# Kernel tuning notes

Hardware: AMD Instinct MI355X
Metric: run time of the kernel (lower is better)

Reference implementation:

```python
import jax, jax.numpy as jnp
import numpy as np

NUM_HEADS = 8
GROUP = 16
LN_EPS = 1e-5

def _star_relu(x, scale, bias):
    return scale * jnp.square(jax.nn.relu(x)) + bias

def _layernorm(x, w, b):
    mu = x.mean(-1, keepdims=True)
    var = jnp.mean(jnp.square(x - mu), -1, keepdims=True)
    return (x - mu) / jnp.sqrt(var + LN_EPS) * w + b

def _attention(x, qkv_w, proj_w, proj_b, pa_scale, pa_bias, lf_w, lf_b, hf_w, hf_b, lf_gamma, hf_gamma):
    B, N, C = x.shape
    hd = C // NUM_HEADS
    detail = _star_relu(x, pa_scale, pa_bias)
    lf = jnp.tanh(detail @ lf_w.T + lf_b)                      # (B,N,H)
    hf = jax.nn.softplus(detail @ hf_w.T + hf_b)
    hf_sq = jnp.square(hf)
    hf = 2.0 * hf_sq / (hf_sq + 0.3678)
    lf = jnp.repeat(lf, hd, axis=-1)                           # (B,N,C): per-head value repeated across head_dim
    hf = jnp.repeat(hf, hd, axis=-1)
    qkv = (x @ qkv_w.T).reshape(B, N, 3, NUM_HEADS, hd).transpose(2, 0, 3, 1, 4)
    q, k, v = qkv[0], qkv[1], qkv[2]
    q = q * (hd ** -0.5)
    attn = jax.nn.softmax(jnp.einsum('bhqd,bhkd->bhqk', q, k), axis=-1)
    attn_out = jnp.einsum('bhqk,bhkd->bhqd', attn, v).transpose(0, 2, 1, 3).reshape(B, N, C)
    value_tokens = v.transpose(0, 2, 1, 3).reshape(B, N, C)
    high_res = value_tokens - attn_out
    attn_out = attn_out + attn_out * lf * lf_gamma + hf * high_res * hf_gamma
    return attn_out @ proj_w.T + proj_b

def _freq_scale(x, rw1_w, rw1_scale, rw1_bias, rw2_w, freq_w):
    # x: (B,C,H,W); freq_w: (num_filters, C//group, base_size, base_size//2+1) == rfft grid
    B, C, H, W = x.shape
    xf = jnp.fft.rfft2(x, axes=(2, 3), norm='ortho')           # (B,C,fh,fw) complex
    pooled = x.mean(axis=(2, 3))                               # (B,C)
    h = _star_relu(pooled @ rw1_w.T, rw1_scale, rw1_bias)
    routing = jnp.tanh((h @ rw2_w.T).reshape(B, GROUP, -1))    # (B,g,f)
    fh, fw = xf.shape[2], xf.shape[3]
    dyn = jnp.einsum('bgf,fchw->bgchw', routing, freq_w).reshape(B, C, fh, fw)
    xf = xf * dyn
    return jnp.fft.irfft2(xf, s=(H, W), axes=(2, 3), norm='ortho')

def _forward(x, norm1_w, norm1_b, qkv_w, proj_w, proj_b, pa_scale, pa_bias, lf_w, lf_b, hf_w, hf_b,
             lf_gamma, hf_gamma, fs1_rw1_w, fs1_rw1_scale, fs1_rw1_bias, fs1_rw2_w, fs1_fw, gamma_1,
             norm2_w, norm2_b, fc1_w, fc1_b, fc2_w, fc2_b, fs2_rw1_w, fs2_rw1_scale, fs2_rw1_bias,
             fs2_rw2_w, fs2_fw, gamma_2):
    B, C, H, W = x.shape
    tokens = x.reshape(B, C, H * W).transpose(0, 2, 1)         # nchw -> nlc
    att_tokens = _attention(_layernorm(tokens, norm1_w, norm1_b),
                            qkv_w, proj_w, proj_b, pa_scale, pa_bias,
                            lf_w, lf_b, hf_w, hf_b, lf_gamma, hf_gamma)
    att_feat = att_tokens.transpose(0, 2, 1).reshape(B, C, H, W)
    att_feat = _freq_scale(att_feat, fs1_rw1_w, fs1_rw1_scale, fs1_rw1_bias, fs1_rw2_w, fs1_fw) + att_feat
    att_tokens = att_feat.reshape(B, C, H * W).transpose(0, 2, 1)
    tokens = tokens + gamma_1 * att_tokens
    h = _layernorm(tokens, norm2_w, norm2_b)
    mlp_tokens = jax.nn.gelu(h @ fc1_w.T + fc1_b, approximate=False) @ fc2_w.T + fc2_b
    mlp_feat = mlp_tokens.transpose(0, 2, 1).reshape(B, C, H, W)
    mlp_feat = _freq_scale(mlp_feat, fs2_rw1_w, fs2_rw1_scale, fs2_rw1_bias, fs2_rw2_w, fs2_fw) + mlp_feat
    mlp_tokens = mlp_feat.reshape(B, C, H * W).transpose(0, 2, 1)
    tokens = tokens + gamma_2 * mlp_tokens
    return tokens.transpose(0, 2, 1).reshape(B, C, H, W)

def setup_inputs() -> dict:
    key = jax.random.key(0)
    ks = jax.random.split(key, 16)
    B, C, H, W = 16, 512, 32, 32
    heads, group, nf, bs = 8, 16, 4, 32
    hid_rw = int(C * 0.125)
    hid_mlp = int(C * 4.0)
    bfs = bs // 2 + 1
    d = {}
    d['x'] = jax.random.normal(ks[0], (B, C, H, W), jnp.float32)
    d['norm1_w'] = jnp.ones((C,), jnp.float32); d['norm1_b'] = jnp.zeros((C,), jnp.float32)
    d['qkv_w'] = jax.random.normal(ks[1], (3 * C, C), jnp.float32) * 0.02
    d['proj_w'] = jax.random.normal(ks[2], (C, C), jnp.float32) * 0.02
    d['proj_b'] = jnp.zeros((C,), jnp.float32)
    d['pa_scale'] = jnp.ones((1,), jnp.float32); d['pa_bias'] = jnp.zeros((1,), jnp.float32)
    d['lf_w'] = jax.random.normal(ks[3], (heads, C), jnp.float32) * 0.02
    d['lf_b'] = jnp.zeros((heads,), jnp.float32)
    d['hf_w'] = jax.random.normal(ks[4], (heads, C), jnp.float32) * 0.02
    d['hf_b'] = jnp.zeros((heads,), jnp.float32)
    d['lf_gamma'] = 1e-5 * jnp.ones((C,), jnp.float32)
    d['hf_gamma'] = 1e-5 * jnp.ones((C,), jnp.float32)
    d['fs1_rw1_w'] = jax.random.normal(ks[5], (hid_rw, C), jnp.float32) * 0.02
    d['fs1_rw1_scale'] = jnp.ones((1,), jnp.float32); d['fs1_rw1_bias'] = jnp.zeros((1,), jnp.float32)
    d['fs1_rw2_w'] = jax.random.normal(ks[6], (group * nf, hid_rw), jnp.float32) * 0.02
    d['fs1_fw'] = jax.random.normal(ks[7], (nf, C // group, bs, bfs), jnp.float32) * 1e-5
    d['gamma_1'] = 1e-4 * jnp.ones((C,), jnp.float32)
    d['norm2_w'] = jnp.ones((C,), jnp.float32); d['norm2_b'] = jnp.zeros((C,), jnp.float32)
    d['fc1_w'] = jax.random.normal(ks[8], (hid_mlp, C), jnp.float32) * 0.02
    d['fc1_b'] = jnp.zeros((hid_mlp,), jnp.float32)
    d['fc2_w'] = jax.random.normal(ks[9], (C, hid_mlp), jnp.float32) * 0.02
    d['fc2_b'] = jnp.zeros((C,), jnp.float32)
    d['fs2_rw1_w'] = jax.random.normal(ks[10], (hid_rw, C), jnp.float32) * 0.02
    d['fs2_rw1_scale'] = jnp.ones((1,), jnp.float32); d['fs2_rw1_bias'] = jnp.zeros((1,), jnp.float32)
    d['fs2_rw2_w'] = jax.random.normal(ks[11], (group * nf, hid_rw), jnp.float32) * 0.02
    d['fs2_fw'] = jax.random.normal(ks[12], (nf, C // group, bs, bfs), jnp.float32) * 1e-5
    d['gamma_2'] = 1e-4 * jnp.ones((C,), jnp.float32)
    return d

def reference(x, norm1_w, norm1_b, qkv_w, proj_w, proj_b, pa_scale, pa_bias, lf_w, lf_b, hf_w, hf_b,
              lf_gamma, hf_gamma, fs1_rw1_w, fs1_rw1_scale, fs1_rw1_bias, fs1_rw2_w, fs1_fw, gamma_1,
              norm2_w, norm2_b, fc1_w, fc1_b, fc2_w, fc2_b, fs2_rw1_w, fs2_rw1_scale, fs2_rw1_bias,
              fs2_rw2_w, fs2_fw, gamma_2):
    return _forward(x, norm1_w, norm1_b, qkv_w, proj_w, proj_b, pa_scale, pa_bias, lf_w, lf_b, hf_w, hf_b,
                    lf_gamma, hf_gamma, fs1_rw1_w, fs1_rw1_scale, fs1_rw1_bias, fs1_rw2_w, fs1_fw, gamma_1,
                    norm2_w, norm2_b, fc1_w, fc1_b, fc2_w, fc2_b, fs2_rw1_w, fs2_rw1_scale, fs2_rw1_bias,
                    fs2_rw2_w, fs2_fw, gamma_2)
```

## Files before the change

kernel.cpp:

```cpp
#include <hip/hip_runtime.h>
#include <cstdint>
#include <cstddef>

#define B_   16
#define C_   512
#define N_   1024
#define M_   (B_*N_)
#define NH_  8
#define HD_  64
#define C3_  1536
#define CH_  2048

typedef __attribute__((ext_vector_type(8))) short bf16x8;
typedef __attribute__((ext_vector_type(4))) float f32x4;
typedef __attribute__((ext_vector_type(4))) unsigned short u16x4;

__device__ __forceinline__ unsigned short f2bf(float f) {
  union { float f; unsigned u; } v; v.f = f;
  unsigned r = v.u + 0x7fffu + ((v.u >> 16) & 1u);
  return (unsigned short)(r >> 16);
}
__device__ __forceinline__ float bf2f(unsigned short h) {
  union { unsigned u; float f; } v; v.u = ((unsigned)h) << 16;
  return v.f;
}
__device__ __forceinline__ unsigned f2u(float f) {
  union { float f; unsigned u; } v; v.f = f; return v.u;
}

#define GL16(gp, lp) \
  __builtin_amdgcn_global_load_lds( \
      (const __attribute__((address_space(1))) unsigned int*)(const void*)(gp), \
      (__attribute__((address_space(3))) unsigned int*)(void*)(lp), 16, 0, 0)

__global__ __launch_bounds__(256) void k_f2b4(
    const float* __restrict__ s0, unsigned short* __restrict__ d0,
    const float* __restrict__ s1, unsigned short* __restrict__ d1,
    const float* __restrict__ s2, unsigned short* __restrict__ d2,
    const float* __restrict__ s3, unsigned short* __restrict__ d3) {
  int blk = blockIdx.x, t = threadIdx.x;
  const float* s; unsigned short* d; int off;
  if (blk < 3072)      { s = s0; d = d0; off = blk * 256; }
  else if (blk < 4096) { s = s1; d = d1; off = (blk - 3072) * 256; }
  else if (blk < 8192) { s = s2; d = d2; off = (blk - 4096) * 256; }
  else                 { s = s3; d = d3; off = (blk - 8192) * 256; }
  int i = off + t;
  d[i] = f2bf(s[i]);
}

__global__ __launch_bounds__(256) void k_twid(unsigned short* __restrict__ gtab) {
  int idx = blockIdx.x * 256 + threadIdx.x;
  if (idx >= 6400) return;
  int tab = idx / 1280, rem = idx % 1280;
  int i = rem / 40, j = rem % 40;
  float v = 0.f;
  if (j < 32) {
    float th = 0.19634954084936207f * (float)((i * j) & 31);
    float s, c;
    __sincosf(th, &s, &c);
    if (tab == 0) v = c;
    else if (tab == 1) v = s;
    else if (tab == 2) v = -s;
    else {
      float wg = (j == 0 || j == 16) ? 1.f : 2.f;
      if (j >= 17) wg = 0.f;
      v = (tab == 3) ? wg * c : -wg * s;
    }
  }
  gtab[idx] = f2bf(v);
}

template<bool WITH>
__global__ __launch_bounds__(256) void k_lnt(const float* __restrict__ src,
    const float* __restrict__ w, const float* __restrict__ bia,
    const float* __restrict__ lfw, const float* __restrict__ lfb,
    const float* __restrict__ hfw, const float* __restrict__ hfb,
    const float* __restrict__ pa_s, const float* __restrict__ pa_b,
    unsigned short* __restrict__ lnout, float* __restrict__ lfout,
    float* __restrict__ hfout) {
  __shared__ unsigned short s[512 * 34];
  const int t = threadIdx.x, wv = t >> 6, l = t & 63;
  const int n0 = blockIdx.x * 32, b = blockIdx.y;
  const int cl = t >> 3;
  const int nn = (t & 7) * 4;
  #pragma unroll
  for (int k = 0; k < 16; ++k) {
    int c = k * 32 + cl;
    float4 v = *(const float4*)&src[(size_t)(b * C_ + c) * N_ + n0 + nn];
    s[c * 34 + nn]     = f2bf(v.x);
    s[c * 34 + nn + 1] = f2bf(v.y);
    s[c * 34 + nn + 2] = f2bf(v.z);
    s[c * 34 + nn + 3] = f2bf(v.w);
  }
  __syncthreads();
  float wv8[8], bv8[8];
  #pragma unroll
  for (int k = 0; k < 8; ++k) { wv8[k] = w[l + 64 * k]; bv8[k] = bia[l + 64 * k]; }
  float ps = 1.f, pb = 0.f;
  if (WITH) { ps = pa_s[0]; pb = pa_b[0]; }
  for (int ri = 0; ri < 8; ++ri) {
    const int n = wv * 8 + ri;
    const int row = b * N_ + n0 + n;
    float v[8];
    #pragma unroll
    for (int k = 0; k < 8; ++k) v[k] = bf2f(s[(l + 64 * k) * 34 + n]);
    float sm = 0.f, q = 0.f;
    #pragma unroll
    for (int k = 0; k < 8; ++k) { sm += v[k]; q += v[k] * v[k]; }
    #pragma unroll
    for (int off = 1; off < 64; off <<= 1) { sm += __shfl_xor(sm, off); q += __shfl_xor(q, off); }
    float mu = sm * (1.f / 512.f);
    float var = q * (1.f / 512.f) - mu * mu;
    float rstd = rsqrtf(var + 1e-5f);
    float ln[8];
    #pragma unroll
    for (int k = 0; k < 8; ++k) ln[k] = (v[k] - mu) * rstd * wv8[k] + bv8[k];
    #pragma unroll
    for (int k = 0; k < 8; ++k)
      lnout[(size_t)row * C_ + l + 64 * k] = f2bf(ln[k]);
    if (WITH) {
      float d[8];
      #pragma unroll
      for (int k = 0; k < 8; ++k) { float r = fmaxf(ln[k], 0.f); d[k] = ps * r * r + pb; }
      float lacc[8], hacc[8];
      #pragma unroll
      for (int h = 0; h < 8; ++h) {
        float la = 0.f, ha = 0.f;
        #pragma unroll
        for (int k = 0; k < 8; ++k) {
          la += d[k] * lfw[h * C_ + l + 64 * k];
          ha += d[k] * hfw[h * C_ + l + 64 * k];
        }
        lacc[h] = la; hacc[h] = ha;
      }
      #pragma unroll
      for (int h = 0; h < 8; ++h)
        #pragma unroll
        for (int off = 1; off < 64; off <<= 1) {
          lacc[h] += __shfl_xor(lacc[h], off);
          hacc[h] += __shfl_xor(hacc[h], off);
        }
      float lv = lacc[0], hv = hacc[0];
      #pragma unroll
      for (int h = 1; h < 8; ++h) { if (l == h) { lv = lacc[h]; hv = hacc[h]; } }
      if (l < 8) {
        lfout[(size_t)row * 8 + l] = tanhf(lv + lfb[l]);
        float z = hv + hfb[l];
        float sp = (z > 15.f) ? z : log1pf(__expf(z));
        float s2 = sp * sp;
        hfout[(size_t)row * 8 + l] = 2.f * s2 / (s2 + 0.3678f);
      }
    }
  }
}

template<int EPI>
__global__ __launch_bounds__(256) void k_gemm(const unsigned short* __restrict__ A,
    const unsigned short* __restrict__ Bt, const float* __restrict__ bias,
    void* __restrict__ outv, unsigned short* __restrict__ vtg, int Nn, int K, int nx) {
  __shared__ __align__(16) unsigned short Asm[128 * 32];
  __shared__ __align__(16) unsigned short Bsm[128 * 32];
  const int t = threadIdx.x, w = t >> 6, l = t & 63;
  const int lane15 = l & 15, quad = l >> 4;
  const int cpx = gridDim.x >> 3;
  const int wgs = (blockIdx.x & 7) * cpx + (blockIdx.x >> 3);
  const int bx = wgs % nx, by = wgs / nx;
  const int n0 = bx * 128, m0 = by * 128;
  const int wm = w >> 1, wn = w & 1;
  f32x4 acc[4][4];
  #pragma unroll
  for (int i = 0; i < 4; ++i)
    #pragma unroll
    for (int j = 0; j < 4; ++j) acc[i][j] = (f32x4){0.f, 0.f, 0.f, 0.f};
  const int srow = w * 16 + (l >> 2);
  const int scol = (l & 3) * 8;
  const unsigned short* gA = A + (size_t)(m0 + srow) * K + scol;
  const unsigned short* gB = Bt + (size_t)(n0 + srow) * K + scol;
  const size_t rk64 = (size_t)64 * K;
  char* lA0 = (char*)Asm + w * 1024;
  char* lA1 = (char*)Asm + 4096 + w * 1024;
  char* lB0 = (char*)Bsm + w * 1024;
  char* lB1 = (char*)Bsm + 4096 + w * 1024;
  for (int k0 = 0; k0 < K; k0 += 32) {
    __syncthreads();
    GL16(gA + k0, lA0);
    GL16(gA + k0 + rk64, lA1);
    GL16(gB + k0, lB0);
    GL16(gB + k0 + rk64, lB1);
    __syncthreads();
    bf16x8 af[4], bg[4];
    #pragma unroll
    for (int i = 0; i < 4; ++i)
      af[i] = *(const bf16x8*)&Asm[(wm * 64 + i * 16 + lane15) * 32 + quad * 8];
    #pragma unroll
    for (int i = 0; i < 4; ++i)
      bg[i] = *(const bf16x8*)&Bsm[(wn * 64 + i * 16 + lane15) * 32 + quad * 8];
    #pragma unroll
    for (int i = 0; i < 4; ++i)
      #pragma unroll
      for (int j = 0; j < 4; ++j)
        acc[i][j] = __builtin_amdgcn_mfma_f32_16x16x32_bf16(af[i], bg[j], acc[i][j], 0, 0, 0);
  }
  #pragma unroll
  for (int i = 0; i < 4; ++i) {
    int grow = m0 + wm * 64 + i * 16 + quad * 4;
    int bq = grow >> 10, nq = grow & 1023;
    #pragma unroll
    for (int j = 0; j < 4; ++j) {
      int gcol = n0 + wn * 64 + j * 16 + lane15;
      float bs = (EPI == 0) ? 0.f : bias[gcol];
      if (EPI == 1 || EPI == 3) {
        float4 o = make_float4(acc[i][j][0] + bs, acc[i][j][1] + bs,
                               acc[i][j][2] + bs, acc[i][j][3] + bs);
        *(float4*)&((float*)outv)[((size_t)(bq * C_ + gcol) << 10) + nq] = o;
      } else if (EPI == 0) {
        u16x4 pv;
        #pragma unroll
        for (int r = 0; r < 4; ++r) {
          unsigned short hv = f2bf(acc[i][j][r]);
          pv[r] = hv;
          ((unsigned short*)outv)[(size_t)(grow + r) * Nn + gcol] = hv;
        }
        if (gcol >= 1024)
          *(u16x4*)&vtg[((size_t)(bq * C_ + gcol - 1024) << 10) + nq] = pv;
      } else {
        #pragma unroll
        for (int r = 0; r < 4; ++r) {
          float vv = acc[i][j][r] + bs;
          float e = __builtin_amdgcn_exp2f(-(2.302118073f * vv +
                                             0.1029455568f * vv * vv * vv));
          float g = vv * __builtin_amdgcn_rcpf(1.f + e);
          ((unsigned short*)outv)[(size_t)(grow + r) * Nn + gcol] = f2bf(g);
        }
      }
    }
  }
}

__global__ __launch_bounds__(256, 4) void k_flash(const unsigned short* __restrict__ qkv,
    const unsigned short* __restrict__ vtg, const float* __restrict__ lf,
    const float* __restrict__ hf, const float* __restrict__ lgam,
    const float* __restrict__ hgam, unsigned short* __restrict__ y) {
  const int t = threadIdx.x, w = t >> 6, l = t & 63;
  const int lane15 = l & 15, quad = l >> 4;
  const int wg = (blockIdx.x & 7) * 128 + (blockIdx.x >> 3);
  const int qt = wg & 7;
  const int h = (wg >> 3) & 7;
  const int b = wg >> 6;
  const int q0 = qt * 128;

  __shared__ __align__(16) unsigned short kt[64 * 64];
  __shared__ __align__(16) unsigned short vt[64 * 64];
  __shared__ __align__(16) unsigned short pl[4][16 * 72];

  bf16x8 aq[2][2];
  #pragma unroll
  for (int qh = 0; qh < 2; ++qh) {
    const unsigned short* qp = qkv +
        (size_t)(b * N_ + q0 + w * 32 + qh * 16 + lane15) * C3_ + h * 64 + quad * 8;
    bf16x8 r0 = *(const bf16x8*)qp;
    bf16x8 r1 = *(const bf16x8*)(qp + 32);
    #pragma unroll
    for (int i = 0; i < 8; ++i) {
      aq[qh][0][i] = (short)f2bf(0.1803368801111713f * bf2f((unsigned short)r0[i]));
      aq[qh][1][i] = (short)f2bf(0.1803368801111713f * bf2f((unsigned short)r1[i]));
    }
  }
  f32x4 O[2][4];
  #pragma unroll
  for (int qh = 0; qh < 2; ++qh)
    #pragma unroll
    for (int i = 0; i < 4; ++i) O[qh][i] = (f32x4){0.f, 0.f, 0.f, 0.f};
  float lsum[2] = {0.f, 0.f};

  const int prow = w * 8 + (l >> 3);
  const int csw = ((l & 7) ^ (l >> 3)) * 8;
  const unsigned short* kg = qkv + (size_t)(b * N_ + prow) * C3_ + 512 + h * 64 + csw;
  const unsigned short* vg = vtg + (size_t)((b * NH_ + h) * HD_ + prow) * N_ + csw;
  char* ktb0 = (char*)kt + w * 1024;
  char* ktb1 = (char*)kt + 4096 + w * 1024;
  char* vtb0 = (char*)vt + w * 1024;
  char* vtb1 = (char*)vt + 4096 + w * 1024;
  const int swx = (lane15 & 7) * 8;

  for (int kti = 0; kti < 16; ++kti) {
    __syncthreads();
    const unsigned short* kr = kg + (size_t)(kti * 64) * C3_;
    GL16(kr, ktb0);
    GL16(kr + (size_t)32 * C3_, ktb1);
    const unsigned short* vr = vg + kti * 64;
    GL16(vr, vtb0);
    GL16(vr + 32 * N_, vtb1);
    __syncthreads();

    #pragma unroll
    for (int qh = 0; qh < 2; ++qh) {
      f32x4 S[4];
      __builtin_amdgcn_s_setprio(1);
      #pragma unroll
      for (int nt = 0; nt < 4; ++nt) {
        const int nrow = nt * 16 + lane15;
        bf16x8 ak0 = *(const bf16x8*)&kt[nrow * 64 + ((quad * 8) ^ swx)];
        bf16x8 ak1 = *(const bf16x8*)&kt[nrow * 64 + ((32 + quad * 8) ^ swx)];
        f32x4 z = (f32x4){0.f, 0.f, 0.f, 0.f};
        z = __builtin_amdgcn_mfma_f32_16x16x32_bf16(ak0, aq[qh][0], z, 0, 0, 0);
        z = __builtin_amdgcn_mfma_f32_16x16x32_bf16(ak1, aq[qh][1], z, 0, 0, 0);
        S[nt] = z;
      }
      __builtin_amdgcn_s_setprio(0);
      #pragma unroll
      for (int nt = 0; nt < 4; ++nt)
        #pragma unroll
        for (int r = 0; r < 4; ++r) {
          float pv = __builtin_amdgcn_exp2f(S[nt][r]);
          S[nt][r] = pv;
          lsum[qh] += pv;
        }
      #pragma unroll
      for (int nt = 0; nt < 4; ++nt) {
        unsigned lo = __builtin_amdgcn_perm(f2u(S[nt][1]), f2u(S[nt][0]), 0x07060302u);
        unsigned hi = __builtin_amdgcn_perm(f2u(S[nt][3]), f2u(S[nt][2]), 0x07060302u);
        *(uint2*)&pl[w][lane15 * 72 + nt * 16 + quad * 4] = make_uint2(lo, hi);
      }
      __builtin_amdgcn_s_setprio(1);
      #pragma unroll
      for (int nc = 0; nc < 2; ++nc) {
        bf16x8 ap = *(const bf16x8*)&pl[w][lane15 * 72 + nc * 32 + quad * 8];
        #pragma unroll
        for (int dt = 0; dt < 4; ++dt) {
          const int vrow = dt * 16 + lane15;
          bf16x8 bv = *(const bf16x8*)&vt[vrow * 64 + ((nc * 32 + quad * 8) ^ swx)];
          O[qh][dt] = __builtin_amdgcn_mfma_f32_16x16x32_bf16(ap, bv, O[qh][dt], 0, 0, 0);
        }
      }
      __builtin_amdgcn_s_setprio(0);
    }
  }

  #pragma unroll
  for (int qh = 0; qh < 2; ++qh) {
    float s = lsum[qh];
    s += __shfl_xor(s, 16);
    s += __shfl_xor(s, 32);
    float inv = 1.f / s;
    float invr[4], lfr[4], hfr[4];
    const size_t rowb = (size_t)(b * N_ + q0 + w * 32 + qh * 16 + quad * 4);
    #pragma unroll
    for (int r = 0; r < 4; ++r) {
      invr[r] = __shfl(inv, quad * 4 + r);
      lfr[r] = lf[(rowb + r) * 8 + h];
      hfr[r] = hf[(rowb + r) * 8 + h];
    }
    #pragma unroll
    for (int dt = 0; dt < 4; ++dt) {
      const int cc = h * 64 + dt * 16 + lane15;
      const float lg = lgam[cc], hg = hgam[cc];
      #pragma unroll
      for (int r = 0; r < 4; ++r) {
        float a = O[qh][dt][r] * invr[r];
        float vval = bf2f(qkv[(rowb + r) * C3_ + 1024 + cc]);
        float res = a + a * lfr[r] * lg + hfr[r] * (vval - a) * hg;
        y[(rowb + r) * C_ + cc] = f2bf(res);
      }
    }
  }
}

__global__ __launch_bounds__(256) void k_pool(const float* __restrict__ feat,
                                              float* __restrict__ pooled) {
  int row = blockIdx.x * 4 + (threadIdx.x >> 6);
  int l = threadIdx.x & 63;
  const float4* p = (const float4*)(feat + (size_t)row * N_);
  float4 a = p[l], b4 = p[l + 64], c4 = p[l + 128], d4 = p[l + 192];
  float s = a.x + a.y + a.z + a.w + b4.x + b4.y + b4.z + b4.w +
            c4.x + c4.y + c4.z + c4.w + d4.x + d4.y + d4.z + d4.w;
  #pragma unroll
  for (int off = 1; off < 64; off <<= 1) s += __shfl_xor(s, off);
  if (l == 0) pooled[row] = s * (1.f / 1024.f);
}

__global__ __launch_bounds__(256) void k_routing(const float* __restrict__ pooled,
    const float* __restrict__ rw1, const float* __restrict__ rw1s,
    const float* __restrict__ rw1b, const float* __restrict__ rw2,
    float* __restrict__ routing) {
  const int b = blockIdx.x, t = threadIdx.x;
  __shared__ float plds[512];
  __shared__ float tile[64][65];
  __shared__ float hl[64];
  plds[t] = pooled[b * 512 + t];
  plds[t + 256] = pooled[b * 512 + t + 256];
  __syncthreads();
  float acc = 0.f;
  for (int c0 = 0; c0 < 512; c0 += 64) {
    #pragma unroll
    for (int kk = 0; kk < 16; ++kk) {
      int idx = kk * 256 + t;
      tile[idx >> 6][idx & 63] = rw1[(size_t)(idx >> 6) * 512 + c0 + (idx & 63)];
    }
    __syncthreads();
    if (t < 64) {
      #pragma unroll
      for (int i = 0; i < 64; ++i) acc += plds[c0 + i] * tile[t][i];
    }
    __syncthreads();
  }
  if (t < 64) {
    float r = fmaxf(acc, 0.f);
    hl[t] = rw1s[0] * r * r + rw1b[0];
  }
  __syncthreads();
  if (t < 64) {
    float r2 = 0.f;
    #pragma unroll
    for (int j = 0; j < 64; ++j) r2 += hl[j] * rw2[(size_t)t * 64 + j];
    routing[b * 64 + t] = tanhf(r2);
  }
}

__global__ __launch_bounds__(256) void k_freq(const float* __restrict__ feat,
    const float* __restrict__ routing, const float* __restrict__ fwtab,
    const unsigned short* __restrict__ gtab, const float* __restrict__ res,
    const float* __restrict__ gamma, float* __restrict__ outp) {
  const int c = blockIdx.x, b = blockIdx.y, t = threadIdx.x;
  const int g = c >> 5, cc = c & 31;
  const int w = t >> 6, l = t & 63;
  const int lane15 = l & 15, quad = l >> 4;
  const int mt = w & 1, nt = w >> 1;
  __shared__ __align__(16) unsigned short Xbf[32 * 40];
  __shared__ __align__(16) float p[32 * 36];
  __shared__ __align__(16) unsigned short Tabs[6400];
  __shared__ __align__(16) unsigned short pl1r[32 * 40], pl1i[32 * 40];
  __shared__ __align__(16) unsigned short pl2r[32 * 40], pl2i[32 * 40];
  __shared__ __align__(16) unsigned short pl3r[32 * 40], pl3i[32 * 40];
  __shared__ float Ms[1024];
  const size_t base = (size_t)(b * C_ + c) * N_;

  {
    float4 v = ((const float4*)(feat + base))[t];
    int hh = t >> 3, w4 = (t & 7) * 4;
    *(float4*)&p[hh * 36 + w4] = v;
    u16x4 xb = { f2bf(v.x), f2bf(v.y), f2bf(v.z), f2bf(v.w) };
    *(u16x4*)&Xbf[hh * 40 + w4] = xb;
  }
  {
    const uint4* src = (const uint4*)gtab;
    uint4* dst = (uint4*)Tabs;
    #pragma unroll
    for (int k = 0; k < 4; ++k) {
      int o = k * 256 + t;
      if (o < 800) dst[o] = src[o];
    }
  }
  {
    float r0 = routing[b * 64 + g * 4 + 0];
    float r1 = routing[b * 64 + g * 4 + 1];
    float r2 = routing[b * 64 + g * 4 + 2];
    float r3 = routing[b * 64 + g * 4 + 3];
    const float* fb = fwtab + (size_t)cc * 544;
    #pragma unroll
    for (int k = 0; k < 4; ++k) {
      int o = k * 256 + t;
      int fh = o >> 5, fw = o & 31;
      float mv = 0.f;
      if (fw < 17) {
        int fi = fh * 17 + fw;
        mv = (r0 * fb[fi] + r1 * fb[17408 + fi] + r2 * fb[34816 + fi] +
              r3 * fb[52224 + fi]) * (1.f / 1024.f);
      }
      Ms[o] = mv;
    }
  }
  __syncthreads();

  const unsigned short* Tc  = Tabs;
  const unsigned short* Ts  = Tabs + 1280;
  const unsigned short* Tsn = Tabs + 2560;
  const unsigned short* Tcw = Tabs + 3840;
  const unsigned short* Tsw = Tabs + 5120;
  const int arow = (mt * 16 + lane15) * 40 + quad * 8;
  const int brow = (nt * 16 + lane15) * 40 + quad * 8;
  const int prow = (nt * 16 + lane15) * 40 + mt * 16 + quad * 4;
  const f32x4 zz = (f32x4){0.f, 0.f, 0.f, 0.f};

  {
    bf16x8 aX = *(const bf16x8*)&Xbf[arow];
    bf16x8 bC = *(const bf16x8*)&Tc[brow];
    bf16x8 bS = *(const bf16x8*)&Tsn[brow];
    f32x4 re = __builtin_amdgcn_mfma_f32_16x16x32_bf16(aX, bC, zz, 0, 0, 0);
    f32x4 im = __builtin_amdgcn_mfma_f32_16x16x32_bf16(aX, bS, zz, 0, 0, 0);
    uint2 pr = make_uint2(__builtin_amdgcn_perm(f2u(re[1]), f2u(re[0]), 0x07060302u),
                          __builtin_amdgcn_perm(f2u(re[3]), f2u(re[2]), 0x07060302u));
    uint2 pi = make_uint2(__builtin_amdgcn_perm(f2u(im[1]), f2u(im[0]), 0x07060302u),
                          __builtin_amdgcn_perm(f2u(im[3]), f2u(im[2]), 0x07060302u));
    *(uint2*)&pl1r[prow] = pr;
    *(uint2*)&pl1i[prow] = pi;
  }
  __syncthreads();
  {
    bf16x8 aC = *(const bf16x8*)&Tc[arow];
    bf16x8 aS = *(const bf16x8*)&Ts[arow];
    bf16x8 aN = *(const bf16x8*)&Tsn[arow];
    bf16x8 bR = *(const bf16x8*)&pl1r[brow];
    bf16x8 bI = *(const bf16x8*)&pl1i[brow];
    f32x4 er = __builtin_amdgcn_mfma_f32_16x16x32_bf16(aC, bR, zz, 0, 0, 0);
    er = __builtin_amdgcn_mfma_f32_16x16x32_bf16(aS, bI, er, 0, 0, 0);
    f32x4 ei = __builtin_amdgcn_mfma_f32_16x16x32_bf16(aC, bI, zz, 0, 0, 0);
    ei = __builtin_amdgcn_mfma_f32_16x16x32_bf16(aN, bR, ei, 0, 0, 0);
    #pragma unroll
    for (int r = 0; r < 4; ++r) {
      float mk = Ms[(mt * 16 + quad * 4 + r) * 32 + nt * 16 + lane15];
      er[r] *= mk; ei[r] *= mk;
    }
    uint2 pr = make_uint2(__builtin_amdgcn_perm(f2u(er[1]), f2u(er[0]), 0x07060302u),
                          __builtin_amdgcn_perm(f2u(er[3]), f2u(er[2]), 0x07060302u));
    uint2 pi = make_uint2(__builtin_amdgcn_perm(f2u(ei[1]), f2u(ei[0]), 0x07060302u),
                          __builtin_amdgcn_perm(f2u(ei[3]), f2u(ei[2]), 0x07060302u));
    *(uint2*)&pl2r[prow] = pr;
    *(uint2*)&pl2i[prow] = pi;
  }
  __syncthreads();
  {
    bf16x8 aR = *(const bf16x8*)&pl2r[arow];
    bf16x8 aI = *(const bf16x8*)&pl2i[arow];
    bf16x8 bC = *(const bf16x8*)&Tc[brow];
    bf16x8 bS = *(const bf16x8*)&Ts[brow];
    bf16x8 bN = *(const bf16x8*)&Tsn[brow];
    f32x4 zr = __builtin_amdgcn_mfma_f32_16x16x32_bf16(aR, bC, zz, 0, 0, 0);
    zr = __builtin_amdgcn_mfma_f32_16x16x32_bf16(aI, bN, zr, 0, 0, 0);
    f32x4 zi = __builtin_amdgcn_mfma_f32_16x16x32_bf16(aI, bC, zz, 0, 0, 0);
    zi = __builtin_amdgcn_mfma_f32_16x16x32_bf16(aR, bS, zi, 0, 0, 0);
    uint2 pr = make_uint2(__builtin_amdgcn_perm(f2u(zr[1]), f2u(zr[0]), 0x07060302u),
                          __builtin_amdgcn_perm(f2u(zr[3]), f2u(zr[2]), 0x07060302u));
    uint2 pi = make_uint2(__builtin_amdgcn_perm(f2u(zi[1]), f2u(zi[0]), 0x07060302u),
                          __builtin_amdgcn_perm(f2u(zi[3]), f2u(zi[2]), 0x07060302u));
    *(uint2*)&pl3r[prow] = pr;
    *(uint2*)&pl3i[prow] = pi;
  }
  __syncthreads();
  {
    bf16x8 aC = *(const bf16x8*)&Tcw[arow];
    bf16x8 aS = *(const bf16x8*)&Tsw[arow];
    bf16x8 bR = *(const bf16x8*)&pl3r[brow];
    bf16x8 bI = *(const bf16x8*)&pl3i[brow];
    f32x4 y = __builtin_amdgcn_mfma_f32_16x16x32_bf16(aC, bR, zz, 0, 0, 0);
    y = __builtin_amdgcn_mfma_f32_16x16x32_bf16(aS, bI, y, 0, 0, 0);
    int hh = nt * 16 + lane15, w0 = mt * 16 + quad * 4;
    float4 fp = *(const float4*)&p[hh * 36 + w0];
    float4 rp = *(const float4*)&res[base + hh * 32 + w0];
    float gv = gamma[c];
    float4 o = make_float4(rp.x + gv * (y[0] + fp.x), rp.y + gv * (y[1] + fp.y),
                           rp.z + gv * (y[2] + fp.z), rp.w + gv * (y[3] + fp.w));
    *(float4*)&outp[base + hh * 32 + w0] = o;
  }
}

extern "C" void kernel_launch(void* const* d_in, const int* in_sizes, int n_in,
                              void* d_out, int out_size, void* d_ws, size_t ws_size,
                              hipStream_t stream) {
  (void)in_sizes; (void)n_in; (void)out_size; (void)ws_size;
  const float* x      = (const float*)d_in[0];
  const float* n1w    = (const float*)d_in[1];
  const float* n1b    = (const float*)d_in[2];
  const float* qkv_w  = (const float*)d_in[3];
  const float* proj_w = (const float*)d_in[4];
  const float* proj_b = (const float*)d_in[5];
  const float* pa_s   = (const float*)d_in[6];
  const float* pa_b   = (const float*)d_in[7];
  const float* lf_w   = (const float*)d_in[8];
  const float* lf_b   = (const float*)d_in[9];
  const float* hf_w   = (const float*)d_in[10];
  const float* hf_b   = (const float*)d_in[11];
  const float* lf_g   = (const float*)d_in[12];
  const float* hf_g   = (const float*)d_in[13];
  const float* f1rw1w = (const float*)d_in[14];
  const float* f1rw1s = (const float*)d_in[15];
  const float* f1rw1b = (const float*)d_in[16];
  const float* f1rw2w = (const float*)d_in[17];
  const float* f1fw   = (const float*)d_in[18];
  const float* gamma1 = (const float*)d_in[19];
  const float* n2w    = (const float*)d_in[20];
  const float* n2b    = (const float*)d_in[21];
  const float* fc1w   = (const float*)d_in[22];
  const float* fc1b   = (const float*)d_in[23];
  const float* fc2w   = (const float*)d_in[24];
  const float* fc2b   = (const float*)d_in[25];
  const float* f2rw1w = (const float*)d_in[26];
  const float* f2rw1s = (const float*)d_in[27];
  const float* f2rw1b = (const float*)d_in[28];
  const float* f2rw2w = (const float*)d_in[29];
  const float* f2fw   = (const float*)d_in[30];
  const float* gamma2 = (const float*)d_in[31];

  char* ws = (char*)d_ws;
  float*          tokens = (float*)(ws + 0);
  float*          f1buf  = (float*)(ws + 33554432ULL);
  float*          f2buf  = (float*)(ws + 67108864ULL);
  unsigned short* regA   = (unsigned short*)(ws + 134217728ULL);
  unsigned short* abuf   = (unsigned short*)(ws + 201326592ULL);
  float*          lfbuf  = (float*)(ws + 218103808ULL);
  float*          hfbuf  = (float*)(ws + 218628096ULL);
  float*          pooled = (float*)(ws + 219152384ULL);
  float*          routing= (float*)(ws + 219185152ULL);
  unsigned short* wq     = (unsigned short*)(ws + 219189248ULL);
  unsigned short* wp     = (unsigned short*)(ws + 220762112ULL);
  unsigned short* w1     = (unsigned short*)(ws + 221286400ULL);
  unsigned short* w2     = (unsigned short*)(ws + 223383552ULL);
  unsigned short* gtab   = (unsigned short*)(ws + 225480704ULL);
  unsigned short* vtg    = (unsigned short*)f1buf;

  k_f2b4<<<12288, 256, 0, stream>>>(qkv_w, wq, proj_w, wp, fc1w, w1, fc2w, w2);
  k_twid<<<25, 256, 0, stream>>>(gtab);

  k_lnt<true><<<dim3(32, 16), 256, 0, stream>>>(x, n1w, n1b, lf_w, lf_b, hf_w, hf_b,
                                                pa_s, pa_b, abuf, lfbuf, hfbuf);
  k_gemm<0><<<1536, 256, 0, stream>>>(abuf, wq, n1b, regA, vtg, C3_, C_, 12);
  k_flash<<<1024, 256, 0, stream>>>(regA, vtg, lfbuf, hfbuf, lf_g, hf_g, abuf);
  k_gemm<1><<<512, 256, 0, stream>>>(abuf, wp, proj_b, f2buf, nullptr, C_, C_, 4);
  k_pool<<<2048, 256, 0, stream>>>(f2buf, pooled);
  k_routing<<<16, 256, 0, stream>>>(pooled, f1rw1w, f1rw1s, f1rw1b, f1rw2w, routing);
  k_freq<<<dim3(512, 16), 256, 0, stream>>>(f2buf, routing, f1fw, gtab, x, gamma1, tokens);
  k_lnt<false><<<dim3(32, 16), 256, 0, stream>>>(tokens, n2w, n2b, nullptr, nullptr,
                                                 nullptr, nullptr, nullptr, nullptr,
                                                 abuf, nullptr, nullptr);
  k_gemm<2><<<2048, 256, 0, stream>>>(abuf, w1, fc1b, regA, nullptr, CH_, C_, 16);
  k_gemm<3><<<512, 256, 0, stream>>>(regA, w2, fc2b, f2buf, nullptr, C_, CH_, 4);
  k_pool<<<2048, 256, 0, stream>>>(f2buf, pooled);
  k_routing<<<16, 256, 0, stream>>>(pooled, f2rw1w, f2rw1s, f2rw1b, f2rw2w, routing);
  k_freq<<<dim3(512, 16), 256, 0, stream>>>(f2buf, routing, f2fw, gtab, tokens, gamma2,
                                            (float*)d_out);
}
```

Before: 513.2 us.

## Double-buffer GEMM and flash LDS tiles, fuse mean-pooling into GEMM epilogue

GEMM and flash-attention loops now keep two LDS buffers and issue the next tile's async global-to-LDS loads before computing on the current one, with a single barrier per iteration. This is meant to overlap memory latency with MFMA work. The P-tile scratch in flash is re-laid out with an XOR swizzle instead of padding. The separate pooling kernels are removed: the proj and fc2 GEMM epilogues accumulate per-column sums and atomically add them into pooled buffers, which the twiddle kernel now zeroes. Doubled LDS may reduce occupancy, and the atomics make the pooled sums order-nondeterministic.

```diff
diff --git a/kernel.cpp b/kernel.cpp
--- a/kernel.cpp
+++ b/kernel.cpp
@@ -48,26 +48,33 @@
   d[i] = f2bf(s[i]);
 }
 
-__global__ __launch_bounds__(256) void k_twid(unsigned short* __restrict__ gtab) {
+__global__ __launch_bounds__(256) void k_twid(unsigned short* __restrict__ gtab,
+                                              float* __restrict__ p1,
+                                              float* __restrict__ p2) {
   int idx = blockIdx.x * 256 + threadIdx.x;
-  if (idx >= 6400) return;
-  int tab = idx / 1280, rem = idx % 1280;
-  int i = rem / 40, j = rem % 40;
-  float v = 0.f;
-  if (j < 32) {
-    float th = 0.19634954084936207f * (float)((i * j) & 31);
-    float s, c;
-    __sincosf(th, &s, &c);
-    if (tab == 0) v = c;
-    else if (tab == 1) v = s;
-    else if (tab == 2) v = -s;
-    else {
-      float wg = (j == 0 || j == 16) ? 1.f : 2.f;
-      if (j >= 17) wg = 0.f;
-      v = (tab == 3) ? wg * c : -wg * s;
-    }
-  }
-  gtab[idx] = f2bf(v);
+  if (idx < 6400) {
+    int tab = idx / 1280, rem = idx % 1280;
+    int i = rem / 40, j = rem % 40;
+    float v = 0.f;
+    if (j < 32) {
+      float th = 0.19634954084936207f * (float)((i * j) & 31);
+      float s, c;
+      __sincosf(th, &s, &c);
+      if (tab == 0) v = c;
+      else if (tab == 1) v = s;
+      else if (tab == 2) v = -s;
+      else {
+        float wg = (j == 0 || j == 16) ? 1.f : 2.f;
+        if (j >= 17) wg = 0.f;
+        v = (tab == 3) ? wg * c : -wg * s;
+      }
+    }
+    gtab[idx] = f2bf(v);
+  } else if (idx < 14592) {
+    p1[idx - 6400] = 0.f;
+  } else if (idx < 22784) {
+    p2[idx - 14592] = 0.f;
+  }
 }
 
 template<bool WITH>
@@ -158,8 +165,8 @@
 __global__ __launch_bounds__(256) void k_gemm(const unsigned short* __restrict__ A,
     const unsigned short* __restrict__ Bt, const float* __restrict__ bias,
     void* __restrict__ outv, unsigned short* __restrict__ vtg, int Nn, int K, int nx) {
-  __shared__ __align__(16) unsigned short Asm[128 * 32];
-  __shared__ __align__(16) unsigned short Bsm[128 * 32];
+  __shared__ __align__(16) unsigned short Asm[2 * 128 * 32];
+  __shared__ __align__(16) unsigned short Bsm[2 * 128 * 32];
   const int t = threadIdx.x, w = t >> 6, l = t & 63;
   const int lane15 = l & 15, quad = l >> 4;
   const int cpx = gridDim.x >> 3;
@@ -177,30 +184,36 @@
   const unsigned short* gA = A + (size_t)(m0 + srow) * K + scol;
   const unsigned short* gB = Bt + (size_t)(n0 + srow) * K + scol;
   const size_t rk64 = (size_t)64 * K;
-  char* lA0 = (char*)Asm + w * 1024;
-  char* lA1 = (char*)Asm + 4096 + w * 1024;
-  char* lB0 = (char*)Bsm + w * 1024;
-  char* lB1 = (char*)Bsm + 4096 + w * 1024;
+  auto stage = [&](int bufi, int k0) {
+    char* a = (char*)Asm + bufi * 8192 + w * 1024;
+    char* bb = (char*)Bsm + bufi * 8192 + w * 1024;
+    GL16(gA + k0, a);
+    GL16(gA + k0 + rk64, a + 4096);
+    GL16(gB + k0, bb);
+    GL16(gB + k0 + rk64, bb + 4096);
+  };
+  stage(0, 0);
+  __syncthreads();
   for (int k0 = 0; k0 < K; k0 += 32) {
-    __syncthreads();
-    GL16(gA + k0, lA0);
-    GL16(gA + k0 + rk64, lA1);
-    GL16(gB + k0, lB0);
-    GL16(gB + k0 + rk64, lB1);
-    __syncthreads();
+    const int cur = (k0 >> 5) & 1;
+    if (k0 + 32 < K) stage(cur ^ 1, k0 + 32);
+    const unsigned short* As = Asm + cur * 4096;
+    const unsigned short* Bs = Bsm + cur * 4096;
     bf16x8 af[4], bg[4];
     #pragma unroll
     for (int i = 0; i < 4; ++i)
-      af[i] = *(const bf16x8*)&Asm[(wm * 64 + i * 16 + lane15) * 32 + quad * 8];
+      af[i] = *(const bf16x8*)&As[(wm * 64 + i * 16 + lane15) * 32 + quad * 8];
     #pragma unroll
     for (int i = 0; i < 4; ++i)
-      bg[i] = *(const bf16x8*)&Bsm[(wn * 64 + i * 16 + lane15) * 32 + quad * 8];
+      bg[i] = *(const bf16x8*)&Bs[(wn * 64 + i * 16 + lane15) * 32 + quad * 8];
     #pragma unroll
     for (int i = 0; i < 4; ++i)
       #pragma unroll
       for (int j = 0; j < 4; ++j)
         acc[i][j] = __builtin_amdgcn_mfma_f32_16x16x32_bf16(af[i], bg[j], acc[i][j], 0, 0, 0);
-  }
+    __syncthreads();
+  }
+  float psum[4] = {0.f, 0.f, 0.f, 0.f};
   #pragma unroll
   for (int i = 0; i < 4; ++i) {
     int grow = m0 + wm * 64 + i * 16 + quad * 4;
@@ -212,6 +225,7 @@
       if (EPI == 1 || EPI == 3) {
         float4 o = make_float4(acc[i][j][0] + bs, acc[i][j][1] + bs,
                                acc[i][j][2] + bs, acc[i][j][3] + bs);
+        psum[j] += o.x + o.y + o.z + o.w;
         *(float4*)&((float*)outv)[((size_t)(bq * C_ + gcol) << 10) + nq] = o;
       } else if (EPI == 0) {
         u16x4 pv;
@@ -235,6 +249,20 @@
       }
     }
   }
+  if (EPI == 1 || EPI == 3) {
+    float* pooled = (float*)vtg;
+    const int bq = m0 >> 10;
+    #pragma unroll
+    for (int j = 0; j < 4; ++j) {
+      float v = psum[j] * (1.f / 1024.f);
+      v += __shfl_xor(v, 16);
+      v += __shfl_xor(v, 32);
+      if (quad == 0) {
+        int gcol = n0 + wn * 64 + j * 16 + lane15;
+        atomicAdd(&pooled[bq * C_ + gcol], v);
+      }
+    }
+  }
 }
 
 __global__ __launch_bounds__(256, 4) void k_flash(const unsigned short* __restrict__ qkv,
@@ -249,9 +277,9 @@
   const int b = wg >> 6;
   const int q0 = qt * 128;
 
-  __shared__ __align__(16) unsigned short kt[64 * 64];
-  __shared__ __align__(16) unsigned short vt[64 * 64];
-  __shared__ __align__(16) unsigned short pl[4][16 * 72];
+  __shared__ __align__(16) unsigned short kt[2 * 64 * 64];
+  __shared__ __align__(16) unsigned short vt[2 * 64 * 64];
+  __shared__ __align__(16) unsigned short pl[4][16 * 64];
 
   bf16x8 aq[2][2];
   #pragma unroll
@@ -277,21 +305,29 @@
   const int csw = ((l & 7) ^ (l >> 3)) * 8;
   const unsigned short* kg = qkv + (size_t)(b * N_ + prow) * C3_ + 512 + h * 64 + csw;
   const unsigned short* vg = vtg + (size_t)((b * NH_ + h) * HD_ + prow) * N_ + csw;
-  char* ktb0 = (char*)kt + w * 1024;
-  char* ktb1 = (char*)kt + 4096 + w * 1024;
-  char* vtb0 = (char*)vt + w * 1024;
-  char* vtb1 = (char*)vt + 4096 + w * 1024;
   const int swx = (lane15 & 7) * 8;
 
+  auto stage = [&](int bufi, int tile) {
+    const unsigned short* kr = kg + (size_t)(tile * 64) * C3_;
+    const unsigned short* vr = vg + tile * 64;
+    char* kb = (char*)kt + bufi * 8192 + w * 1024;
+    char* vb = (char*)vt + bufi * 8192 + w * 1024;
+    GL16(kr, kb);
+    GL16(kr + (size_t)32 * C3_, kb + 4096);
+    GL16(vr, vb);
+    GL16(vr + 32 * N_, vb + 4096);
+  };
+
+  char* plb = (char*)pl[w] + lane15 * 128;
+  const int plx = (lane15 & 7) << 4;
+
+  stage(0, 0);
+  __syncthreads();
+
   for (int kti = 0; kti < 16; ++kti) {
-    __syncthreads();
-    const unsigned short* kr = kg + (size_t)(kti * 64) * C3_;
-    GL16(kr, ktb0);
-    GL16(kr + (size_t)32 * C3_, ktb1);
-    const unsigned short* vr = vg + kti * 64;
-    GL16(vr, vtb0);
-    GL16(vr + 32 * N_, vtb1);
-    __syncthreads();
+    if (kti < 15) stage((kti + 1) & 1, kti + 1);
+    const unsigned short* ktc = kt + (kti & 1) * 4096;
+    const unsigned short* vtc = vt + (kti & 1) * 4096;
 
     #pragma unroll
     for (int qh = 0; qh < 2; ++qh) {
@@ -300,8 +336,8 @@
       #pragma unroll
       for (int nt = 0; nt < 4; ++nt) {
         const int nrow = nt * 16 + lane15;
-        bf16x8 ak0 = *(const bf16x8*)&kt[nrow * 64 + ((quad * 8) ^ swx)];
-        bf16x8 ak1 = *(const bf16x8*)&kt[nrow * 64 + ((32 + quad * 8) ^ swx)];
+        bf16x8 ak0 = *(const bf16x8*)&ktc[nrow * 64 + ((quad * 8) ^ swx)];
+        bf16x8 ak1 = *(const bf16x8*)&ktc[nrow * 64 + ((32 + quad * 8) ^ swx)];
         f32x4 z = (f32x4){0.f, 0.f, 0.f, 0.f};
         z = __builtin_amdgcn_mfma_f32_16x16x32_bf16(ak0, aq[qh][0], z, 0, 0, 0);
         z = __builtin_amdgcn_mfma_f32_16x16x32_bf16(ak1, aq[qh][1], z, 0, 0, 0);
@@ -320,21 +356,22 @@
       for (int nt = 0; nt < 4; ++nt) {
         unsigned lo = __builtin_amdgcn_perm(f2u(S[nt][1]), f2u(S[nt][0]), 0x07060302u);
         unsigned hi = __builtin_amdgcn_perm(f2u(S[nt][3]), f2u(S[nt][2]), 0x07060302u);
-        *(uint2*)&pl[w][lane15 * 72 + nt * 16 + quad * 4] = make_uint2(lo, hi);
+        *(uint2*)(plb + ((nt * 32 + quad * 8) ^ plx)) = make_uint2(lo, hi);
       }
       __builtin_amdgcn_s_setprio(1);
       #pragma unroll
       for (int nc = 0; nc < 2; ++nc) {
-        bf16x8 ap = *(const bf16x8*)&pl[w][lane15 * 72 + nc * 32 + quad * 8];
+        bf16x8 ap = *(const bf16x8*)(plb + ((nc * 64 + quad * 16) ^ plx));
         #pragma unroll
         for (int dt = 0; dt < 4; ++dt) {
           const int vrow = dt * 16 + lane15;
-          bf16x8 bv = *(const bf16x8*)&vt[vrow * 64 + ((nc * 32 + quad * 8) ^ swx)];
+          bf16x8 bv = *(const bf16x8*)&vtc[vrow * 64 + ((nc * 32 + quad * 8) ^ swx)];
           O[qh][dt] = __builtin_amdgcn_mfma_f32_16x16x32_bf16(ap, bv, O[qh][dt], 0, 0, 0);
         }
       }
       __builtin_amdgcn_s_setprio(0);
     }
+    __syncthreads();
   }
 
   #pragma unroll
@@ -364,19 +401,6 @@
       }
     }
   }
-}
-
-__global__ __launch_bounds__(256) void k_pool(const float* __restrict__ feat,
-                                              float* __restrict__ pooled) {
-  int row = blockIdx.x * 4 + (threadIdx.x >> 6);
-  int l = threadIdx.x & 63;
-  const float4* p = (const float4*)(feat + (size_t)row * N_);
-  float4 a = p[l], b4 = p[l + 64], c4 = p[l + 128], d4 = p[l + 192];
-  float s = a.x + a.y + a.z + a.w + b4.x + b4.y + b4.z + b4.w +
-            c4.x + c4.y + c4.z + c4.w + d4.x + d4.y + d4.z + d4.w;
-  #pragma unroll
-  for (int off = 1; off < 64; off <<= 1) s += __shfl_xor(s, off);
-  if (l == 0) pooled[row] = s * (1.f / 1024.f);
 }
 
 __global__ __launch_bounds__(256) void k_routing(const float* __restrict__ pooled,
@@ -607,25 +631,26 @@
   unsigned short* w2     = (unsigned short*)(ws + 223383552ULL);
   unsigned short* gtab   = (unsigned short*)(ws + 225480704ULL);
   unsigned short* vtg    = (unsigned short*)f1buf;
+  float*          pooled2= (float*)(ws + 50331648ULL);
 
   k_f2b4<<<12288, 256, 0, stream>>>(qkv_w, wq, proj_w, wp, fc1w, w1, fc2w, w2);
-  k_twid<<<25, 256, 0, stream>>>(gtab);
+  k_twid<<<89, 256, 0, stream>>>(gtab, pooled, pooled2);
 
   k_lnt<true><<<dim3(32, 16), 256, 0, stream>>>(x, n1w, n1b, lf_w, lf_b, hf_w, hf_b,
                                                 pa_s, pa_b, abuf, lfbuf, hfbuf);
   k_gemm<0><<<1536, 256, 0, stream>>>(abuf, wq, n1b, regA, vtg, C3_, C_, 12);
   k_flash<<<1024, 256, 0, stream>>>(regA, vtg, lfbuf, hfbuf, lf_g, hf_g, abuf);
-  k_gemm<1><<<512, 256, 0, stream>>>(abuf, wp, proj_b, f2buf, nullptr, C_, C_, 4);
-  k_pool<<<2048, 256, 0, stream>>>(f2buf, pooled);
+  k_gemm<1><<<512, 256, 0, stream>>>(abuf, wp, proj_b, f2buf,
+                                     (unsigned short*)pooled, C_, C_, 4);
   k_routing<<<16, 256, 0, stream>>>(pooled, f1rw1w, f1rw1s, f1rw1b, f1rw2w, routing);
   k_freq<<<dim3(512, 16), 256, 0, stream>>>(f2buf, routing, f1fw, gtab, x, gamma1, tokens);
   k_lnt<false><<<dim3(32, 16), 256, 0, stream>>>(tokens, n2w, n2b, nullptr, nullptr,
                                                  nullptr, nullptr, nullptr, nullptr,
                                                  abuf, nullptr, nullptr);
   k_gemm<2><<<2048, 256, 0, stream>>>(abuf, w1, fc1b, regA, nullptr, CH_, C_, 16);
-  k_gemm<3><<<512, 256, 0, stream>>>(regA, w2, fc2b, f2buf, nullptr, C_, CH_, 4);
-  k_pool<<<2048, 256, 0, stream>>>(f2buf, pooled);
-  k_routing<<<16, 256, 0, stream>>>(pooled, f2rw1w, f2rw1s, f2rw1b, f2rw2w, routing);
+  k_gemm<3><<<512, 256, 0, stream>>>(regA, w2, fc2b, f2buf,
+                                     (unsigned short*)pooled2, C_, CH_, 4);
+  k_routing<<<16, 256, 0, stream>>>(pooled2, f2rw1w, f2rw1s, f2rw1b, f2rw2w, routing);
   k_freq<<<dim3(512, 16), 256, 0, stream>>>(f2buf, routing, f2fw, gtab, tokens, gamma2,
                                             (float*)d_out);
 }
```

New measurement: 503.1 us. 1.02x faster.
